# Kernel tuning notes

Hardware: AMD Instinct MI355X
Metric: run time of the kernel (lower is better)

## Reference

```python
import jax, jax.numpy as jnp
import numpy as np

VOCAB = 8192
ZC = 32
BETA = 0.25
EPS = 1e-12  # torch F.normalize eps


def l2norm(x):
    return x / jnp.maximum(jnp.linalg.norm(x, axis=-1, keepdims=True), EPS)


def setup_inputs() -> dict:
    key = jax.random.key(0)
    k1, k2 = jax.random.split(key)
    z = jax.random.normal(k1, (16, ZC, 32, 32), dtype=jnp.float32)  # [B, C, H, W]
    emb = jax.random.uniform(k2, (VOCAB, ZC), dtype=jnp.float32,
                             minval=-1.0 / VOCAB, maxval=1.0 / VOCAB)
    emb = l2norm(emb)  # codebook_norm init
    return {"z": z, "embedding": emb}


def reference(z, embedding):
    # b c h w -> b h w c
    zc = jnp.einsum('bchw->bhwc', z)
    z_flat = zc.reshape(-1, ZC)                      # [N, C], N = B*H*W
    # codebook_norm: normalize inputs and codebook
    z_flat = l2norm(z_flat)
    zn = z_flat.reshape(zc.shape)                    # normalized z, [B,H,W,C]
    e = l2norm(embedding)                            # [V, C]
    # squared euclidean distances: ||z||^2 + ||e||^2 - 2 z e^T  -> [N, V]
    d = (jnp.sum(z_flat ** 2, axis=1, keepdims=True)
         + jnp.sum(e ** 2, axis=1)
         - 2.0 * jnp.einsum('nd,vd->nv', z_flat, e))
    idx = jnp.argmin(d, axis=1)                      # [N]
    z_q = l2norm(embedding[idx]).reshape(zc.shape)   # gather + normalize
    commit_loss = BETA * jnp.mean((jax.lax.stop_gradient(z_q) - zn) ** 2)
    vq_loss = jnp.mean((z_q - jax.lax.stop_gradient(zn)) ** 2)
    # straight-through estimator
    z_q = zn + jax.lax.stop_gradient(z_q - zn)
    z_q = jnp.einsum('bhwc->bchw', z_q)
    return z_q, vq_loss, commit_loss
```

## Files before the change

kernel.cpp:

```cpp
#include <hip/hip_runtime.h>

typedef _Float16 f16;
typedef _Float16 f16x8 __attribute__((ext_vector_type(8)));
typedef float f32x4 __attribute__((ext_vector_type(4)));

#define ZC 32
#define HW 1024
#define TPB 256
#define VCH 512
#define ZROWS_BLK 256

__device__ __forceinline__ unsigned int fkey(float x) {
    unsigned int b = __float_as_uint(x);
    return (b & 0x80000000u) ? ~b : (b | 0x80000000u);
}

__global__ void kprep_e(const float* __restrict__ emb, float* __restrict__ e,
                        f16* __restrict__ Eh, f16* __restrict__ El, int V) {
    int r = blockIdx.x * blockDim.x + threadIdx.x;
    if (r >= V) return;
    const float4* src = reinterpret_cast<const float4*>(emb) + (size_t)r * 8;
    float4 v[8];
    float s = 0.f;
#pragma unroll
    for (int j = 0; j < 8; ++j) {
        v[j] = src[j];
        s += v[j].x * v[j].x + v[j].y * v[j].y + v[j].z * v[j].z + v[j].w * v[j].w;
    }
    float inv = 1.0f / fmaxf(sqrtf(s), 1e-12f);
    float4* dst = reinterpret_cast<float4*>(e) + (size_t)r * 8;
    f16* eh = Eh + (size_t)r * ZC;
    f16* el = El + (size_t)r * ZC;
#pragma unroll
    for (int j = 0; j < 8; ++j) {
        float t0 = v[j].x * inv, t1 = v[j].y * inv, t2 = v[j].z * inv, t3 = v[j].w * inv;
        float4 o; o.x = t0; o.y = t1; o.z = t2; o.w = t3;
        dst[j] = o;
        f16 h0 = (f16)t0, h1 = (f16)t1, h2 = (f16)t2, h3 = (f16)t3;
        eh[4 * j + 0] = h0; eh[4 * j + 1] = h1; eh[4 * j + 2] = h2; eh[4 * j + 3] = h3;
        el[4 * j + 0] = (f16)(t0 - (float)h0);
        el[4 * j + 1] = (f16)(t1 - (float)h1);
        el[4 * j + 2] = (f16)(t2 - (float)h2);
        el[4 * j + 3] = (f16)(t3 - (float)h3);
    }
}

__global__ void kprep_z(const float* __restrict__ z, f16x8* __restrict__ ZFh,
                        f16x8* __restrict__ ZFl, int N) {
    int t = blockIdx.x * blockDim.x + threadIdx.x;
    if (t >= N * 4) return;
    int lane = t & 63, zt = t >> 6;
    int n = zt * 16 + (lane & 15);
    int b = n >> 10, hw = n & 1023;
    int kb = (lane >> 4) * 8;
    f16x8 h, l;
#pragma unroll
    for (int j = 0; j < 8; ++j) {
        float v = z[((size_t)(b * ZC + kb + j)) * HW + hw];
        f16 hh = (f16)v;
        h[j] = hh;
        l[j] = (f16)(v - (float)hh);
    }
    ZFh[t] = h;
    ZFl[t] = l;
}

__global__ __launch_bounds__(TPB, 2) void kmfma(const f16x8* __restrict__ ZFh,
                                                const f16x8* __restrict__ ZFl,
                                                const uint4* __restrict__ Eh,
                                                const uint4* __restrict__ El,
                                                unsigned long long* __restrict__ packed,
                                                int Vm1) {
    __shared__ uint4 sEh[VCH * 4];
    __shared__ uint4 sEl[VCH * 4];
    const int tid = threadIdx.x;
    const int cb = blockIdx.x & 15;
    const int zb = blockIdx.x >> 4;

    {
        const uint4* gh = Eh + (size_t)cb * (VCH * 4);
        const uint4* gl = El + (size_t)cb * (VCH * 4);
#pragma unroll
        for (int i = 0; i < 8; ++i) {
            int c = tid + i * TPB;
            int r = c >> 2, q = c & 3;
            int w = (r << 2) | (q ^ ((r >> 1) & 3));
            sEh[w] = gh[c];
            sEl[w] = gl[c];
        }
    }

    const int lane = tid & 63;
    const int wv = tid >> 6;
    const int zt0 = zb * 16 + wv * 4;

    f16x8 Bh[4], Bl[4];
#pragma unroll
    for (int i = 0; i < 4; ++i) {
        Bh[i] = ZFh[(size_t)(zt0 + i) * 64 + lane];
        Bl[i] = ZFl[(size_t)(zt0 + i) * 64 + lane];
    }
    __syncthreads();

    const int r15 = lane & 15, qq = lane >> 4;
    const int laneA = (r15 << 2) | (qq ^ ((r15 >> 1) & 3));

    float bv[4] = {-1e38f, -1e38f, -1e38f, -1e38f};
    int bi[4] = {0, 0, 0, 0};
    int g = cb * VCH + qq * 4;

    for (int ct = 0; ct < VCH / 16; ++ct) {
        f16x8 Ah = *(const f16x8*)&sEh[ct * 64 + laneA];
        f16x8 Al = *(const f16x8*)&sEl[ct * 64 + laneA];
#pragma unroll
        for (int i = 0; i < 4; ++i) {
            f32x4 acc = {0.f, 0.f, 0.f, 0.f};
            acc = __builtin_amdgcn_mfma_f32_16x16x32_f16(Ah, Bh[i], acc, 0, 0, 0);
            acc = __builtin_amdgcn_mfma_f32_16x16x32_f16(Ah, Bl[i], acc, 0, 0, 0);
            acc = __builtin_amdgcn_mfma_f32_16x16x32_f16(Al, Bh[i], acc, 0, 0, 0);
#pragma unroll
            for (int r = 0; r < 4; ++r) {
                float v = acc[r];
                bool gt = v > bv[i];
                bi[i] = gt ? (g + r) : bi[i];
                bv[i] = gt ? v : bv[i];
            }
        }
        g += 16;
    }

#pragma unroll
    for (int i = 0; i < 4; ++i) {
        unsigned long long key =
            ((unsigned long long)fkey(bv[i]) << 32) | (unsigned int)(Vm1 - bi[i]);
        unsigned long long o;
        o = __shfl_xor(key, 16); if (o > key) key = o;
        o = __shfl_xor(key, 32); if (o > key) key = o;
        if (lane < 16) atomicMax(&packed[(size_t)(zt0 + i) * 16 + r15], key);
    }
}

__global__ void kfinal(const float* __restrict__ z, const float* __restrict__ e,
                       const unsigned long long* __restrict__ packed,
                       float* __restrict__ out, float* __restrict__ partial, int V) {
    __shared__ float red[TPB];
    int n = blockIdx.x * TPB + threadIdx.x;
    int b = n >> 10, hw = n & 1023;
    unsigned long long p = packed[n];
    int idx = (V - 1) - (int)(unsigned int)(p & 0xFFFFFFFFull);

    float zrow[ZC];
    float s = 0.f;
#pragma unroll
    for (int c = 0; c < ZC; ++c) {
        float t = z[((size_t)b * ZC + c) * HW + hw];
        zrow[c] = t;
        s += t * t;
    }
    float inv = 1.0f / fmaxf(sqrtf(s), 1e-12f);

    const float4* er = reinterpret_cast<const float4*>(e) + (size_t)idx * 8;
    float loss = 0.f;
#pragma unroll
    for (int q = 0; q < 8; ++q) {
        float4 ev = er[q];
        float d0 = ev.x - zrow[4 * q + 0] * inv;
        float d1 = ev.y - zrow[4 * q + 1] * inv;
        float d2 = ev.z - zrow[4 * q + 2] * inv;
        float d3 = ev.w - zrow[4 * q + 3] * inv;
        loss += d0 * d0 + d1 * d1 + d2 * d2 + d3 * d3;
        out[((size_t)b * ZC + (4 * q + 0)) * HW + hw] = ev.x;
        out[((size_t)b * ZC + (4 * q + 1)) * HW + hw] = ev.y;
        out[((size_t)b * ZC + (4 * q + 2)) * HW + hw] = ev.z;
        out[((size_t)b * ZC + (4 * q + 3)) * HW + hw] = ev.w;
    }

    red[threadIdx.x] = loss;
    __syncthreads();
    for (int st = TPB / 2; st > 0; st >>= 1) {
        if (threadIdx.x < st) red[threadIdx.x] += red[threadIdx.x + st];
        __syncthreads();
    }
    if (threadIdx.x == 0) partial[blockIdx.x] = red[0];
}

__global__ void kloss(const float* __restrict__ partial, float* __restrict__ out,
                      int nblocks, int NC) {
    if (blockIdx.x == 0 && threadIdx.x == 0) {
        float s = 0.f;
        for (int i = 0; i < nblocks; ++i) s += partial[i];
        float mean = s / (float)NC;
        out[NC] = mean;
        out[NC + 1] = 0.25f * mean;
    }
}

extern "C" void kernel_launch(void* const* d_in, const int* in_sizes, int n_in,
                              void* d_out, int out_size, void* d_ws, size_t ws_size,
                              hipStream_t stream) {
    const float* z = (const float*)d_in[0];
    const float* emb = (const float*)d_in[1];
    float* out = (float*)d_out;

    const int N = in_sizes[0] / ZC;
    const int V = in_sizes[1] / ZC;

    char* ws = (char*)d_ws;
    float* e = (float*)ws;
    f16* Eh = (f16*)(ws + (size_t)V * ZC * 4);
    f16* El = (f16*)(ws + (size_t)V * ZC * 6);
    f16x8* ZFh = (f16x8*)(ws + (size_t)V * ZC * 8);
    f16x8* ZFl = (f16x8*)(ws + (size_t)V * ZC * 8 + (size_t)N * ZC * 2);
    unsigned long long* packed =
        (unsigned long long*)(ws + (size_t)V * ZC * 8 + (size_t)N * ZC * 4);
    float* partial = (float*)((char*)packed + (size_t)N * 8);

    hipMemsetAsync(packed, 0, (size_t)N * 8, stream);
    kprep_e<<<(V + TPB - 1) / TPB, TPB, 0, stream>>>(emb, e, Eh, El, V);
    kprep_z<<<(N * 4 + TPB - 1) / TPB, TPB, 0, stream>>>(z, ZFh, ZFl, N);
    kmfma<<<(V / VCH) * (N / ZROWS_BLK), TPB, 0, stream>>>(
        ZFh, ZFl, (const uint4*)Eh, (const uint4*)El, packed, V - 1);
    kfinal<<<N / TPB, TPB, 0, stream>>>(z, e, packed, out, partial, V);
    kloss<<<1, 64, 0, stream>>>(partial, out, N / TPB, N * ZC);
}
```

Before: 52.79 us.

## Fuse prep kernels and memset, halve codebook chunk, parallelize loss reduction

Merges the z and codebook prep kernels and the packed-buffer memset into one launch, cutting two launches and a memset. Halves the codebook chunk per MFMA block (VCH 512→256), which doubles the grid to 2048 blocks, halves LDS use and raises launch bounds to 4 blocks/SM for more occupancy. It also reorders block indexing so z-tiles vary fastest, and replaces the serial single-thread final loss sum with a wave shuffle reduction. In exchange, each z-tile's B fragments are reloaded twice as often and twice as many atomics are issued.

```diff
diff --git a/kernel.cpp b/kernel.cpp
--- a/kernel.cpp
+++ b/kernel.cpp
@@ -7,7 +7,7 @@
 #define ZC 32
 #define HW 1024
 #define TPB 256
-#define VCH 512
+#define VCH 256
 #define ZROWS_BLK 256
 
 __device__ __forceinline__ unsigned int fkey(float x) {
@@ -15,57 +15,64 @@
     return (b & 0x80000000u) ? ~b : (b | 0x80000000u);
 }
 
-__global__ void kprep_e(const float* __restrict__ emb, float* __restrict__ e,
-                        f16* __restrict__ Eh, f16* __restrict__ El, int V) {
-    int r = blockIdx.x * blockDim.x + threadIdx.x;
-    if (r >= V) return;
-    const float4* src = reinterpret_cast<const float4*>(emb) + (size_t)r * 8;
-    float4 v[8];
-    float s = 0.f;
-#pragma unroll
-    for (int j = 0; j < 8; ++j) {
-        v[j] = src[j];
-        s += v[j].x * v[j].x + v[j].y * v[j].y + v[j].z * v[j].z + v[j].w * v[j].w;
-    }
-    float inv = 1.0f / fmaxf(sqrtf(s), 1e-12f);
-    float4* dst = reinterpret_cast<float4*>(e) + (size_t)r * 8;
-    f16* eh = Eh + (size_t)r * ZC;
-    f16* el = El + (size_t)r * ZC;
-#pragma unroll
-    for (int j = 0; j < 8; ++j) {
-        float t0 = v[j].x * inv, t1 = v[j].y * inv, t2 = v[j].z * inv, t3 = v[j].w * inv;
-        float4 o; o.x = t0; o.y = t1; o.z = t2; o.w = t3;
-        dst[j] = o;
-        f16 h0 = (f16)t0, h1 = (f16)t1, h2 = (f16)t2, h3 = (f16)t3;
-        eh[4 * j + 0] = h0; eh[4 * j + 1] = h1; eh[4 * j + 2] = h2; eh[4 * j + 3] = h3;
-        el[4 * j + 0] = (f16)(t0 - (float)h0);
-        el[4 * j + 1] = (f16)(t1 - (float)h1);
-        el[4 * j + 2] = (f16)(t2 - (float)h2);
-        el[4 * j + 3] = (f16)(t3 - (float)h3);
-    }
-}
-
-__global__ void kprep_z(const float* __restrict__ z, f16x8* __restrict__ ZFh,
-                        f16x8* __restrict__ ZFl, int N) {
-    int t = blockIdx.x * blockDim.x + threadIdx.x;
-    if (t >= N * 4) return;
-    int lane = t & 63, zt = t >> 6;
-    int n = zt * 16 + (lane & 15);
-    int b = n >> 10, hw = n & 1023;
-    int kb = (lane >> 4) * 8;
-    f16x8 h, l;
-#pragma unroll
-    for (int j = 0; j < 8; ++j) {
-        float v = z[((size_t)(b * ZC + kb + j)) * HW + hw];
-        f16 hh = (f16)v;
-        h[j] = hh;
-        l[j] = (f16)(v - (float)hh);
-    }
-    ZFh[t] = h;
-    ZFl[t] = l;
-}
-
-__global__ __launch_bounds__(TPB, 2) void kmfma(const f16x8* __restrict__ ZFh,
+__global__ void kprep(const float* __restrict__ z, const float* __restrict__ emb,
+                      float* __restrict__ e, f16* __restrict__ Eh, f16* __restrict__ El,
+                      f16x8* __restrict__ ZFh, f16x8* __restrict__ ZFl,
+                      unsigned long long* __restrict__ packed,
+                      int N, int V, int zblocks) {
+    const int blk = blockIdx.x;
+    if (blk < zblocks) {
+        int t = blk * TPB + threadIdx.x;
+        if (t < N * 4) {
+            int lane = t & 63, zt = t >> 6;
+            int n = zt * 16 + (lane & 15);
+            int b = n >> 10, hw = n & 1023;
+            int kb = (lane >> 4) * 8;
+            f16x8 h, l;
+#pragma unroll
+            for (int j = 0; j < 8; ++j) {
+                float v = z[((size_t)(b * ZC + kb + j)) * HW + hw];
+                f16 hh = (f16)v;
+                h[j] = hh;
+                l[j] = (f16)(v - (float)hh);
+            }
+            ZFh[t] = h;
+            ZFl[t] = l;
+        }
+        int per = (N + zblocks - 1) / zblocks;
+        int p0 = blk * per + threadIdx.x;
+        if (threadIdx.x < per && p0 < N) packed[p0] = 0ull;
+    } else {
+        int r = (blk - zblocks) * TPB + threadIdx.x;
+        if (r >= V) return;
+        const float4* src = reinterpret_cast<const float4*>(emb) + (size_t)r * 8;
+        float4 v[8];
+        float s = 0.f;
+#pragma unroll
+        for (int j = 0; j < 8; ++j) {
+            v[j] = src[j];
+            s += v[j].x * v[j].x + v[j].y * v[j].y + v[j].z * v[j].z + v[j].w * v[j].w;
+        }
+        float inv = 1.0f / fmaxf(sqrtf(s), 1e-12f);
+        float4* dst = reinterpret_cast<float4*>(e) + (size_t)r * 8;
+        f16* eh = Eh + (size_t)r * ZC;
+        f16* el = El + (size_t)r * ZC;
+#pragma unroll
+        for (int j = 0; j < 8; ++j) {
+            float t0 = v[j].x * inv, t1 = v[j].y * inv, t2 = v[j].z * inv, t3 = v[j].w * inv;
+            float4 o; o.x = t0; o.y = t1; o.z = t2; o.w = t3;
+            dst[j] = o;
+            f16 h0 = (f16)t0, h1 = (f16)t1, h2 = (f16)t2, h3 = (f16)t3;
+            eh[4 * j + 0] = h0; eh[4 * j + 1] = h1; eh[4 * j + 2] = h2; eh[4 * j + 3] = h3;
+            el[4 * j + 0] = (f16)(t0 - (float)h0);
+            el[4 * j + 1] = (f16)(t1 - (float)h1);
+            el[4 * j + 2] = (f16)(t2 - (float)h2);
+            el[4 * j + 3] = (f16)(t3 - (float)h3);
+        }
+    }
+}
+
+__global__ __launch_bounds__(TPB, 4) void kmfma(const f16x8* __restrict__ ZFh,
                                                 const f16x8* __restrict__ ZFl,
                                                 const uint4* __restrict__ Eh,
                                                 const uint4* __restrict__ El,
@@ -74,14 +81,14 @@
     __shared__ uint4 sEh[VCH * 4];
     __shared__ uint4 sEl[VCH * 4];
     const int tid = threadIdx.x;
-    const int cb = blockIdx.x & 15;
-    const int zb = blockIdx.x >> 4;
+    const int zb = blockIdx.x & 63;
+    const int cb = blockIdx.x >> 6;
 
     {
         const uint4* gh = Eh + (size_t)cb * (VCH * 4);
         const uint4* gl = El + (size_t)cb * (VCH * 4);
 #pragma unroll
-        for (int i = 0; i < 8; ++i) {
+        for (int i = 0; i < 4; ++i) {
             int c = tid + i * TPB;
             int r = c >> 2, q = c & 3;
             int w = (r << 2) | (q ^ ((r >> 1) & 3));
@@ -186,9 +193,11 @@
 
 __global__ void kloss(const float* __restrict__ partial, float* __restrict__ out,
                       int nblocks, int NC) {
-    if (blockIdx.x == 0 && threadIdx.x == 0) {
-        float s = 0.f;
-        for (int i = 0; i < nblocks; ++i) s += partial[i];
+    int lane = threadIdx.x;
+    float s = (lane < nblocks) ? partial[lane] : 0.f;
+#pragma unroll
+    for (int off = 32; off > 0; off >>= 1) s += __shfl_down(s, off);
+    if (lane == 0) {
         float mean = s / (float)NC;
         out[NC] = mean;
         out[NC + 1] = 0.25f * mean;
@@ -215,9 +224,11 @@
         (unsigned long long*)(ws + (size_t)V * ZC * 8 + (size_t)N * ZC * 4);
     float* partial = (float*)((char*)packed + (size_t)N * 8);
 
-    hipMemsetAsync(packed, 0, (size_t)N * 8, stream);
-    kprep_e<<<(V + TPB - 1) / TPB, TPB, 0, stream>>>(emb, e, Eh, El, V);
-    kprep_z<<<(N * 4 + TPB - 1) / TPB, TPB, 0, stream>>>(z, ZFh, ZFl, N);
+    const int zblocks = (N * 4 + TPB - 1) / TPB;
+    const int eblocks = (V + TPB - 1) / TPB;
+
+    kprep<<<zblocks + eblocks, TPB, 0, stream>>>(z, emb, e, Eh, El, ZFh, ZFl,
+                                                 packed, N, V, zblocks);
     kmfma<<<(V / VCH) * (N / ZROWS_BLK), TPB, 0, stream>>>(
         ZFh, ZFl, (const uint4*)Eh, (const uint4*)El, packed, V - 1);
     kfinal<<<N / TPB, TPB, 0, stream>>>(z, e, packed, out, partial, V);
```

Result: faster. 42.29 us (-19.9%).
